# Kernel tuning notes

Measured on AMD Instinct MI355X. Metric: run time of the kernel, lower is better.

The kernel has to match this reference:

```python
import jax, jax.numpy as jnp
import numpy as np

HIDDEN = 2048
N_HEADS = 16
HEAD_DIM = HIDDEN // N_HEADS  # 128
KV_DIM = HEAD_DIM             # multi_query: 1 kv head
INTER = 4 * HIDDEN
EPS = 1e-5


def setup_inputs() -> dict:
    key = jax.random.key(0)
    ks = jax.random.split(key, 16)
    s = 0.02
    d = dict(
        hidden_states=jax.random.normal(ks[0], (4, 2048, HIDDEN), jnp.float32),
        ln1_g=jnp.ones((HIDDEN,), jnp.float32),
        ln1_b=jnp.zeros((HIDDEN,), jnp.float32),
        ln2_g=jnp.ones((HIDDEN,), jnp.float32),
        ln2_b=jnp.zeros((HIDDEN,), jnp.float32),
        wq=jax.random.normal(ks[1], (HIDDEN, HIDDEN), jnp.float32) * s,
        bq=jnp.zeros((HIDDEN,), jnp.float32),
        wkv=jax.random.normal(ks[2], (HIDDEN, 2 * KV_DIM), jnp.float32) * s,
        bkv=jnp.zeros((2 * KV_DIM,), jnp.float32),
        wo=jax.random.normal(ks[3], (HIDDEN, HIDDEN), jnp.float32) * s,
        bo=jnp.zeros((HIDDEN,), jnp.float32),
        wfc=jax.random.normal(ks[4], (HIDDEN, INTER), jnp.float32) * s,
        bfc=jnp.zeros((INTER,), jnp.float32),
        wproj=jax.random.normal(ks[5], (INTER, HIDDEN), jnp.float32) * s,
        bproj=jnp.zeros((HIDDEN,), jnp.float32),
    )
    return d


def _ln(x, g, b):
    m = jnp.mean(x, -1, keepdims=True)
    v = jnp.var(x, -1, keepdims=True)
    return (x - m) * jax.lax.rsqrt(v + EPS) * g + b


def _block(x, ln1_g, ln1_b, ln2_g, ln2_b, wq, bq, wkv, bkv, wo, bo, wfc, bfc, wproj, bproj):
    B, S, H = x.shape
    scale = HEAD_DIM ** -0.5
    # --- attention ---
    res = x
    h = _ln(x, ln1_g, ln1_b)
    q = (h @ wq + bq).reshape(B, S, N_HEADS, HEAD_DIM)
    kv = h @ wkv + bkv                       # [B,S,2*KV_DIM]
    k, v = kv[..., :KV_DIM], kv[..., KV_DIM:]  # [B,S,D] single kv head (MQA)
    scores = jnp.einsum('bshd,btd->bhst', q, k) * scale
    causal = jnp.tril(jnp.ones((S, S), bool))
    scores = jnp.where(causal, scores, jnp.finfo(scores.dtype).min)
    probs = jax.nn.softmax(scores, axis=-1)
    attn = jnp.einsum('bhst,btd->bshd', probs, v).reshape(B, S, H)
    x = attn @ wo + bo + res
    # --- mlp ---
    res = x
    h = _ln(x, ln2_g, ln2_b)
    h = jax.nn.gelu(h @ wfc + bfc, approximate=True)  # gelu_pytorch_tanh
    return h @ wproj + bproj + res


def reference(hidden_states, ln1_g, ln1_b, ln2_g, ln2_b, wq, bq, wkv, bkv, wo, bo, wfc, bfc, wproj, bproj):
    return _block(hidden_states, ln1_g, ln1_b, ln2_g, ln2_b, wq, bq, wkv, bkv, wo, bo, wfc, bfc, wproj, bproj)
```

## Files before the change

### kernel.cpp

```cpp
#include <hip/hip_runtime.h>
#include <hip/hip_bf16.h>
#include <math.h>

typedef __bf16 bf16;
typedef __bf16 bf16x8 __attribute__((ext_vector_type(8)));
typedef float  f32x4  __attribute__((ext_vector_type(4)));

#define HID    2048
#define INTER_ 8192
#define SEQ    2048
#define NTOK   8192
#define HD     128

__device__ __forceinline__ f32x4 mfma16(bf16x8 a, bf16x8 b, f32x4 c){
  return __builtin_amdgcn_mfma_f32_16x16x32_bf16(a, b, c, 0, 0, 0);
}

__device__ __forceinline__ void gl_lds16(const void* g, void* l){
  __builtin_amdgcn_global_load_lds((const __attribute__((address_space(1))) void*)g,
                                   (__attribute__((address_space(3))) void*)l,
                                   16, 0, 0);
}

__global__ __launch_bounds__(256)
void convT_k(const float* __restrict__ in, bf16* __restrict__ out, int K, int N)
{
  __shared__ float tile[32][33];
  const int k0 = blockIdx.x * 32, n0 = blockIdx.y * 32;
  const int tx = threadIdx.x & 31, ty = threadIdx.x >> 5;
#pragma unroll
  for (int r = 0; r < 4; r++)
    tile[ty + r*8][tx] = in[(size_t)(k0 + ty + r*8) * N + n0 + tx];
  __syncthreads();
#pragma unroll
  for (int r = 0; r < 4; r++)
    out[(size_t)(n0 + ty + r*8) * K + k0 + tx] = (bf16)tile[tx][ty + r*8];
}

__global__ __launch_bounds__(256)
void ln_k(const float* __restrict__ x, const float* __restrict__ gamma,
          const float* __restrict__ beta, bf16* __restrict__ out)
{
  const int row = blockIdx.x, t = threadIdx.x;
  const float* xr = x + (size_t)row * HID;
  const float4 a = ((const float4*)xr)[t*2];
  const float4 b = ((const float4*)xr)[t*2 + 1];
  float s  = a.x+a.y+a.z+a.w + b.x+b.y+b.z+b.w;
  float ss = a.x*a.x+a.y*a.y+a.z*a.z+a.w*a.w + b.x*b.x+b.y*b.y+b.z*b.z+b.w*b.w;
#pragma unroll
  for (int m = 32; m; m >>= 1){ s += __shfl_xor(s, m); ss += __shfl_xor(ss, m); }
  __shared__ float red[8];
  const int w = t >> 6;
  if ((t & 63) == 0){ red[w*2] = s; red[w*2+1] = ss; }
  __syncthreads();
  s  = red[0] + red[2] + red[4] + red[6];
  ss = red[1] + red[3] + red[5] + red[7];
  const float mean = s * (1.0f/HID);
  const float var  = ss * (1.0f/HID) - mean*mean;
  const float rs   = rsqrtf(var + 1e-5f);
  const int c = t * 8;
  const float xe[8] = {a.x,a.y,a.z,a.w,b.x,b.y,b.z,b.w};
  bf16x8 o;
#pragma unroll
  for (int e = 0; e < 8; e++)
    o[e] = (bf16)((xe[e] - mean) * rs * gamma[c+e] + beta[c+e]);
  *(bf16x8*)(out + (size_t)row*HID + c) = o;
}

template<int EPI>
__global__ __launch_bounds__(256)
void gemm_bt(const bf16* __restrict__ A, const bf16* __restrict__ BT,
             int M, int N, int K,
             const float* __restrict__ bias, const float* __restrict__ bias2,
             const float* __restrict__ res, float* __restrict__ outf,
             bf16* __restrict__ o0, bf16* __restrict__ o1, bf16* __restrict__ o2)
{
  __shared__ bf16 lA[128*32];
  __shared__ bf16 lB[128*32];
  const int t = threadIdx.x, l = t & 63, w = t >> 6;
  int bx = blockIdx.x, by = blockIdx.y;
  {
    const int nwg = gridDim.x * gridDim.y;
    if ((nwg & 7) == 0){
      int wg = by * gridDim.x + bx;
      const int per = nwg >> 3;
      wg = (wg & 7) * per + (wg >> 3);
      bx = wg % gridDim.x; by = wg / gridDim.x;
    }
  }
  const int m0 = bx * 128, n0 = by * 128;
  const int wm = (w >> 1) * 64, wn = (w & 1) * 64;
  const int g16 = l >> 4, c16 = l & 15;
  const f32x4 z4 = {0.f, 0.f, 0.f, 0.f};
  f32x4 acc[4][4];
#pragma unroll
  for (int i = 0; i < 4; i++)
#pragma unroll
    for (int j = 0; j < 4; j++) acc[i][j] = z4;

  const int srow = (t * 16) >> 6;
  const int scol = ((t * 16) & 63) >> 1;

  for (int k0 = 0; k0 < K; k0 += 32){
    __syncthreads();
    gl_lds16(A  + (size_t)(m0 + srow)      * K + k0 + scol, (char*)lA + t*16);
    gl_lds16(A  + (size_t)(m0 + 64 + srow) * K + k0 + scol, (char*)lA + 4096 + t*16);
    gl_lds16(BT + (size_t)(n0 + srow)      * K + k0 + scol, (char*)lB + t*16);
    gl_lds16(BT + (size_t)(n0 + 64 + srow) * K + k0 + scol, (char*)lB + 4096 + t*16);
    __syncthreads();
    bf16x8 af[4], bfv[4];
#pragma unroll
    for (int i = 0; i < 4; i++){
      af[i]  = *(const bf16x8*)&lA[(wm + i*16 + c16)*32 + g16*8];
      bfv[i] = *(const bf16x8*)&lB[(wn + i*16 + c16)*32 + g16*8];
    }
#pragma unroll
    for (int i = 0; i < 4; i++)
#pragma unroll
      for (int j = 0; j < 4; j++)
        acc[i][j] = mfma16(af[i], bfv[j], acc[i][j]);
  }

#pragma unroll
  for (int i = 0; i < 4; i++)
#pragma unroll
    for (int j = 0; j < 4; j++)
#pragma unroll
      for (int r = 0; r < 4; r++){
        const int row = m0 + wm + i*16 + g16*4 + r;
        const int col = n0 + wn + j*16 + c16;
        const float v = acc[i][j][r];
        if constexpr (EPI == 0){
          if (col < HID){
            o0[(size_t)row*HID + col] = (bf16)(v + bias[col]);
          } else {
            const int nn = col - HID;
            const float vv = v + bias2[nn];
            if (nn < HD) o1[(size_t)row*HD + nn] = (bf16)vv;
            else {
              const int d = nn - HD;
              o2[((size_t)(row >> 11)*HD + d)*SEQ + (row & (SEQ-1))] = (bf16)vv;
            }
          }
        } else if constexpr (EPI == 1){
          outf[(size_t)row*HID + col] = v + bias[col] + res[(size_t)row*HID + col];
        } else if constexpr (EPI == 2){
          const float u = v + bias[col];
          const float a2 = 1.5957691216057308f * (u + 0.044715f*u*u*u);
          const float th = 1.0f - 2.0f/(__expf(a2) + 1.0f);
          o0[(size_t)row*INTER_ + col] = (bf16)(0.5f * u * (1.0f + th));
        } else {
          float* op = outf + (size_t)row*HID + col;
          *op = v + bias[col] + *op;
        }
      }
}

__global__ __launch_bounds__(256)
void attn_k(const bf16* __restrict__ qbuf, const bf16* __restrict__ kb,
            const bf16* __restrict__ vT, bf16* ob)
{
  __shared__ bf16 pl[4][16][64];
  const int bid0 = blockIdx.x;
  const int bid = ((bid0 & 7) << 7) + (bid0 >> 3);
  const int b  = bid >> 8;
  const int h  = (bid >> 4) & 15;
  const int pr = bid & 15;
  const int t = threadIdx.x, w = t >> 6, l = t & 63;
  const int g16 = l >> 4, c16 = l & 15;
  const float scale = 0.08838834764831845f;
  const f32x4 z4 = {0.f,0.f,0.f,0.f};
  const bf16* kbase = kb + (size_t)b*SEQ*HD;
  const bf16* vbase = vT + (size_t)b*HD*SEQ;

#pragma unroll
  for (int pass = 0; pass < 2; pass++){
    const int qb_i = pass ? (31 - pr) : pr;
    const int q0 = qb_i * 64;
    const bf16* qrow = qbuf + (size_t)(b*SEQ + q0 + w*16 + c16)*HID + h*HD + g16*8;
    bf16x8 qf[4];
#pragma unroll
    for (int dc = 0; dc < 4; dc++) qf[dc] = *(const bf16x8*)(qrow + dc*32);

    f32x4 acc[8];
#pragma unroll
    for (int i = 0; i < 8; i++) acc[i] = z4;
    float mrun[4] = {-1e30f,-1e30f,-1e30f,-1e30f};
    float lrun[4] = {0.f,0.f,0.f,0.f};
    const int qg_ = q0 + w*16 + g16*4;

    for (int kt = 0; kt <= qb_i; kt++){
      const int t0 = kt * 64;
      f32x4 s[4] = {z4, z4, z4, z4};
#pragma unroll
      for (int ks = 0; ks < 4; ks++){
        const bf16* kr = kbase + (size_t)(t0 + ks*16 + c16)*HD + g16*8;
#pragma unroll
        for (int dc = 0; dc < 4; dc++)
          s[ks] = mfma16(qf[dc], *(const bf16x8*)(kr + dc*32), s[ks]);
      }
      bf16x8 v0a[4], v1a[4];
#pragma unroll
      for (int dt = 0; dt < 4; dt++){
        const bf16* vr = vbase + (size_t)(dt*16 + c16)*SEQ + t0 + g16*8;
        v0a[dt] = *(const bf16x8*)vr;
        v1a[dt] = *(const bf16x8*)(vr + 32);
      }
      const bool last = (kt == qb_i);
      float coef[4];
#pragma unroll
      for (int r = 0; r < 4; r++){
        float sv[4];
#pragma unroll
        for (int ks = 0; ks < 4; ks++) sv[ks] = s[ks][r] * scale;
        if (last){
          const int qg = qg_ + r;
#pragma unroll
          for (int ks = 0; ks < 4; ks++)
            if (t0 + ks*16 + c16 > qg) sv[ks] = -1e30f;
        }
        float mv = fmaxf(fmaxf(sv[0], sv[1]), fmaxf(sv[2], sv[3]));
#pragma unroll
        for (int mk = 1; mk < 16; mk <<= 1) mv = fmaxf(mv, __shfl_xor(mv, mk));
        const float mn = fmaxf(mrun[r], mv);
        float p[4], ps = 0.f;
#pragma unroll
        for (int ks = 0; ks < 4; ks++){ p[ks] = __expf(sv[ks] - mn); ps += p[ks]; }
#pragma unroll
        for (int mk = 1; mk < 16; mk <<= 1) ps += __shfl_xor(ps, mk);
        coef[r] = __expf(mrun[r] - mn);
        lrun[r] = lrun[r]*coef[r] + ps;
        mrun[r] = mn;
#pragma unroll
        for (int ks = 0; ks < 4; ks++)
          pl[w][g16*4 + r][ks*16 + c16] = (bf16)p[ks];
      }
#pragma unroll
      for (int dt = 0; dt < 8; dt++)
#pragma unroll
        for (int r = 0; r < 4; r++) acc[dt][r] *= coef[r];
      const bf16x8 pa0 = *(const bf16x8*)&pl[w][c16][g16*8];
      const bf16x8 pa1 = *(const bf16x8*)&pl[w][c16][32 + g16*8];
#pragma unroll
      for (int dt = 0; dt < 4; dt++){
        acc[dt] = mfma16(pa0, v0a[dt], acc[dt]);
        acc[dt] = mfma16(pa1, v1a[dt], acc[dt]);
      }
#pragma unroll
      for (int dt = 4; dt < 8; dt++){
        const bf16* vr = vbase + (size_t)(dt*16 + c16)*SEQ + t0 + g16*8;
        acc[dt] = mfma16(pa0, *(const bf16x8*)vr,        acc[dt]);
        acc[dt] = mfma16(pa1, *(const bf16x8*)(vr + 32), acc[dt]);
      }
    }
#pragma unroll
    for (int r = 0; r < 4; r++){
      const float inv = 1.0f / lrun[r];
      bf16* orow = ob + (size_t)(b*SEQ + qg_ + r)*HID + h*HD;
#pragma unroll
      for (int dt = 0; dt < 8; dt++)
        orow[dt*16 + c16] = (bf16)(acc[dt][r] * inv);
    }
  }
}

extern "C" void kernel_launch(void* const* d_in, const int* in_sizes, int n_in,
                              void* d_out, int out_size, void* d_ws, size_t ws_size,
                              hipStream_t stream)
{
  const float* x    = (const float*)d_in[0];
  const float* ln1g = (const float*)d_in[1];
  const float* ln1b = (const float*)d_in[2];
  const float* ln2g = (const float*)d_in[3];
  const float* ln2b = (const float*)d_in[4];
  const float* wq   = (const float*)d_in[5];
  const float* bq   = (const float*)d_in[6];
  const float* wkv  = (const float*)d_in[7];
  const float* bkv  = (const float*)d_in[8];
  const float* wo   = (const float*)d_in[9];
  const float* bo   = (const float*)d_in[10];
  const float* wfc  = (const float*)d_in[11];
  const float* bfc  = (const float*)d_in[12];
  const float* wpr  = (const float*)d_in[13];
  const float* bpr  = (const float*)d_in[14];
  float* out = (float*)d_out;
  (void)in_sizes; (void)n_in; (void)out_size; (void)ws_size;

  char* p = (char*)d_ws;
  auto carve = [&](size_t n){ char* r = p; p += (n + 255) & ~(size_t)255; return r; };
  bf16* wqkvT = (bf16*)carve((size_t)2304*2048*2);
  bf16* woT   = (bf16*)carve((size_t)2048*2048*2);
  bf16* wfcT  = (bf16*)carve((size_t)8192*2048*2);
  bf16* wprT  = (bf16*)carve((size_t)2048*8192*2);
  bf16* hbuf  = (bf16*)carve((size_t)NTOK*2048*2);
  bf16* qbuf  = (bf16*)carve((size_t)NTOK*2048*2);
  bf16* kbuf  = (bf16*)carve((size_t)NTOK*128*2);
  bf16* vbufT = (bf16*)carve((size_t)NTOK*128*2);
  const size_t grows = 4096;
  {
    const size_t span = (size_t)(p - (char*)qbuf);
    const size_t need = grows * (size_t)INTER_ * 2;
    if (need > span) carve(need - span);
  }
  bf16* gbuf = qbuf;

  dim3 B(256);
  convT_k<<<dim3(64, 64),  B, 0, stream>>>(wq,  wqkvT, 2048, 2048);
  convT_k<<<dim3(64, 8),   B, 0, stream>>>(wkv, wqkvT + (size_t)2048*2048, 2048, 256);
  convT_k<<<dim3(64, 64),  B, 0, stream>>>(wo,  woT,  2048, 2048);
  convT_k<<<dim3(64, 256), B, 0, stream>>>(wfc, wfcT, 2048, 8192);
  convT_k<<<dim3(256, 64), B, 0, stream>>>(wpr, wprT, 8192, 2048);

  ln_k<<<NTOK, B, 0, stream>>>(x, ln1g, ln1b, hbuf);
  gemm_bt<0><<<dim3(64, 18), B, 0, stream>>>(hbuf, wqkvT, NTOK, 2304, 2048,
                                             bq, bkv, nullptr, nullptr, qbuf, kbuf, vbufT);
  attn_k<<<1024, B, 0, stream>>>(qbuf, kbuf, vbufT, qbuf );
  gemm_bt<1><<<dim3(64, 16), B, 0, stream>>>(qbuf, woT, NTOK, 2048, 2048,
                                             bo, nullptr, x, out, nullptr, nullptr, nullptr);
  ln_k<<<NTOK, B, 0, stream>>>(out, ln2g, ln2b, hbuf);
  for (size_t c = 0; c < NTOK/grows; c++){
    const size_t ro = c * grows;
    gemm_bt<2><<<dim3(grows/128, 64), B, 0, stream>>>(hbuf + ro*HID, wfcT, (int)grows, 8192, 2048,
                                               bfc, nullptr, nullptr, nullptr, gbuf, nullptr, nullptr);
    gemm_bt<3><<<dim3(grows/128, 16), B, 0, stream>>>(gbuf, wprT, (int)grows, 2048, 8192,
                                               bpr, nullptr, nullptr, out + ro*HID, nullptr, nullptr, nullptr);
  }
}
```

Baseline: 1.948 ms.

## Double-buffer K tiles in LDS via async global-to-LDS loads in attention

The attention kernel now stages each 64x128 K tile into a double-buffered, XOR-swizzled shared-memory buffer using global_load_lds, prefetching the next tile while the current one is consumed. Before, each wave read K fragments straight from global memory, so all four waves fetched the same K data redundantly. The change adds a block-wide barrier per key tile and 32KB of LDS, which may reduce occupancy and adds synchronisation cost. V is still read from global memory.

```diff
diff --git a/kernel.cpp b/kernel.cpp
--- a/kernel.cpp
+++ b/kernel.cpp
@@ -160,6 +160,7 @@
 void attn_k(const bf16* __restrict__ qbuf, const bf16* __restrict__ kb,
             const bf16* __restrict__ vT, bf16* ob)
 {
+  __shared__ bf16 lK[2][64][128];
   __shared__ bf16 pl[4][16][64];
   const int bid0 = blockIdx.x;
   const int bid = ((bid0 & 7) << 7) + (bid0 >> 3);
@@ -172,7 +173,23 @@
   const f32x4 z4 = {0.f,0.f,0.f,0.f};
   const bf16* kbase = kb + (size_t)b*SEQ*HD;
   const bf16* vbase = vT + (size_t)b*HD*SEQ;
-
+  const int kswz = (c16 & 7) << 4;
+
+  int srow4[4], scb4[4];
+#pragma unroll
+  for (int i = 0; i < 4; i++){
+    const int slot = i*256 + t;
+    srow4[i] = slot >> 4;
+    scb4[i]  = ((slot & 15) * 16) ^ ((srow4[i] & 7) << 4);
+  }
+  auto stageK = [&](int bsel, int tile0){
+#pragma unroll
+    for (int i = 0; i < 4; i++)
+      gl_lds16((const char*)kbase + ((size_t)(tile0 + srow4[i])*HD)*2 + scb4[i],
+               (char*)lK + bsel*16384 + (i*256 + t)*16);
+  };
+
+  int buf = 0;
 #pragma unroll
   for (int pass = 0; pass < 2; pass++){
     const int qb_i = pass ? (31 - pr) : pr;
@@ -189,15 +206,22 @@
     float lrun[4] = {0.f,0.f,0.f,0.f};
     const int qg_ = q0 + w*16 + g16*4;
 
+    stageK(buf, 0);
+    __syncthreads();
+
     for (int kt = 0; kt <= qb_i; kt++){
       const int t0 = kt * 64;
+      if (kt < qb_i) stageK(buf ^ 1, t0 + 64);
       f32x4 s[4] = {z4, z4, z4, z4};
+      const char* lkb = (const char*)lK + buf*16384;
 #pragma unroll
       for (int ks = 0; ks < 4; ks++){
-        const bf16* kr = kbase + (size_t)(t0 + ks*16 + c16)*HD + g16*8;
-#pragma unroll
-        for (int dc = 0; dc < 4; dc++)
-          s[ks] = mfma16(qf[dc], *(const bf16x8*)(kr + dc*32), s[ks]);
+        const char* krow = lkb + (ks*16 + c16)*256;
+#pragma unroll
+        for (int dc = 0; dc < 4; dc++){
+          const bf16x8 kf = *(const bf16x8*)(krow + ((dc*64 + g16*16) ^ kswz));
+          s[ks] = mfma16(qf[dc], kf, s[ks]);
+        }
       }
       bf16x8 v0a[4], v1a[4];
 #pragma unroll
@@ -252,6 +276,8 @@
         acc[dt] = mfma16(pa0, *(const bf16x8*)vr,        acc[dt]);
         acc[dt] = mfma16(pa1, *(const bf16x8*)(vr + 32), acc[dt]);
       }
+      __syncthreads();
+      buf ^= 1;
     }
 #pragma unroll
     for (int r = 0; r < 4; r++){
```

New measurement: 1.771 ms. 9.1% less time.
